# Optimization experiments

Measured on AMD Instinct MI355X. Metric: run time of the kernel, lower is better.

Reference implementation:

```python
import jax, jax.numpy as jnp
import numpy as np

HEADS = 12

def setup_inputs() -> dict:
    key = jax.random.key(0)
    ks = jax.random.split(key, 6)
    dim = 768
    x  = jax.random.normal(ks[0], (2, 4096, dim), dtype=jnp.float32)
    s = dim ** -0.5
    wq = jax.random.normal(ks[1], (dim, dim), dtype=jnp.float32) * s
    wk = jax.random.normal(ks[2], (dim, dim), dtype=jnp.float32) * s
    wv = jax.random.normal(ks[3], (dim, dim), dtype=jnp.float32) * s
    wo = jax.random.normal(ks[4], (dim, dim), dtype=jnp.float32) * s
    bo = jnp.zeros((dim,), dtype=jnp.float32)
    return {"x": x, "wq": wq, "wk": wk, "wv": wv, "wo": wo, "bo": bo}

def reference(x, wq, wk, wv, wo, bo):
    b, n, dim = x.shape
    h = HEADS
    d = dim // h
    scale = d ** -0.5
    # nn.Linear(dim, dim, bias=False): y = x @ W.T ; weights stored [out, in]
    def proj(w):
        return (x @ w.T).reshape(b, n, h, d).transpose(0, 2, 1, 3)  # b h n d
    q, k, v = proj(wq), proj(wk), proj(wv)
    dots = jnp.einsum('bhqd,bhkd->bhqk', q, k) * scale  # full N x N scores
    attn = jax.nn.softmax(dots, axis=-1)
    out = jnp.einsum('bhqk,bhkd->bhqd', attn, v)
    out = out.transpose(0, 2, 1, 3).reshape(b, n, dim)
    # to_out: Linear(dim, dim) + Dropout (identity at inference)
    return out @ wo.T + bo
```

## Files before the change

### kernel.cpp

```cpp
#include <hip/hip_runtime.h>
#include <hip/hip_bf16.h>


#define HEADS 12
#define NSEQ  4096
#define DIM   768
#define DH    64
#define BATCH 2
#define QSCALE 0.18033688f

typedef __attribute__((ext_vector_type(8))) short bf16x8;
typedef __attribute__((ext_vector_type(4))) float f32x4;
typedef __attribute__((ext_vector_type(4))) short bf16x4;

static __device__ __forceinline__ short f2bf(float f) {
    __hip_bfloat16 h = __float2bfloat16(f);
    return *reinterpret_cast<short*>(&h);
}

static __device__ __forceinline__ unsigned pkbf(float a, float b) {
    unsigned ua = __float_as_uint(a), ub = __float_as_uint(b);
    ua += 0x7FFFu + ((ua >> 16) & 1u);
    ub += 0x7FFFu + ((ub >> 16) & 1u);
    return __builtin_amdgcn_perm(ub, ua, 0x07060302);
}

#define GLL(g, l) __builtin_amdgcn_global_load_lds( \
    (const __attribute__((address_space(1))) void*)(g), \
    (__attribute__((address_space(3))) void*)(l), 16, 0, 0)

#define NX (BATCH*NSEQ*DIM)
#define NW (DIM*DIM)

__global__ __launch_bounds__(256) void convert_kernel(
    const float* __restrict__ x,  const float* __restrict__ wq,
    const float* __restrict__ wk, const float* __restrict__ wv,
    const float* __restrict__ wo,
    short* __restrict__ xb, short* __restrict__ wqb, short* __restrict__ wkb,
    short* __restrict__ wvb, short* __restrict__ wob)
{
    int i = (blockIdx.x * 256 + threadIdx.x) * 4;
    const float* src; short* dst; int off;
    if      (i < NX)          { src = x;  dst = xb;  off = i; }
    else if (i < NX + NW)     { src = wq; dst = wqb; off = i - NX; }
    else if (i < NX + 2*NW)   { src = wk; dst = wkb; off = i - NX - NW; }
    else if (i < NX + 3*NW)   { src = wv; dst = wvb; off = i - NX - 2*NW; }
    else                      { src = wo; dst = wob; off = i - NX - 3*NW; }
    float4 f = *(const float4*)(src + off);
    bf16x4 o; o[0] = f2bf(f.x); o[1] = f2bf(f.y); o[2] = f2bf(f.z); o[3] = f2bf(f.w);
    *(bf16x4*)(dst + off) = o;
}

__global__ __launch_bounds__(256, 4) void qkv_proj_kernel(
    const short* __restrict__ xb, const short* __restrict__ wqb,
    const short* __restrict__ wkb, const short* __restrict__ wvb,
    short* __restrict__ qb, short* __restrict__ kb, short* __restrict__ vtb)
{
    __shared__ __align__(16) short As[2][128*32];
    __shared__ __align__(16) short Bs[2][128*32];

    const int wave = threadIdx.x >> 6, lane = threadIdx.x & 63;
    const int lr = lane & 15, lq = lane >> 4;
    const int which = blockIdx.y / 6;
    const short* __restrict__ W = (which == 0) ? wqb : ((which == 1) ? wkb : wvb);
    const int m0  = blockIdx.x * 128;
    const int o0l = (blockIdx.y % 6) * 128;

    const short* __restrict__ gA = xb + (size_t)(m0  + wave*32 + (lane>>2)) * DIM + (lane&3)*8;
    const short* __restrict__ gB = W  + (size_t)(o0l + wave*32 + (lane>>2)) * DIM + (lane&3)*8;

    const int wm = (wave & 1) * 64, wn = (wave >> 1) * 64;

    f32x4 acc[4][4];
    #pragma unroll
    for (int i = 0; i < 4; i++)
        #pragma unroll
        for (int j = 0; j < 4; j++) acc[i][j] = (f32x4){0.f, 0.f, 0.f, 0.f};

    GLL(gA,            &As[0][(wave*32     )*32]);
    GLL(gA + 16*DIM,   &As[0][(wave*32 + 16)*32]);
    GLL(gB,            &Bs[0][(wave*32     )*32]);
    GLL(gB + 16*DIM,   &Bs[0][(wave*32 + 16)*32]);
    __syncthreads();

    for (int kt = 0; kt < 24; kt++) {
        const int p = kt & 1;
        if (kt < 23) {
            const int k1 = (kt + 1) * 32;
            GLL(gA + k1,          &As[1-p][(wave*32     )*32]);
            GLL(gA + k1 + 16*DIM, &As[1-p][(wave*32 + 16)*32]);
            GLL(gB + k1,          &Bs[1-p][(wave*32     )*32]);
            GLL(gB + k1 + 16*DIM, &Bs[1-p][(wave*32 + 16)*32]);
        }
        bf16x8 a[4], b[4];
        #pragma unroll
        for (int i = 0; i < 4; i++)
            a[i] = *(const bf16x8*)&As[p][(wm + i*16 + lr)*32 + lq*8];
        #pragma unroll
        for (int j = 0; j < 4; j++)
            b[j] = *(const bf16x8*)&Bs[p][(wn + j*16 + lr)*32 + lq*8];
        #pragma unroll
        for (int i = 0; i < 4; i++)
            #pragma unroll
            for (int j = 0; j < 4; j++)
                acc[i][j] = __builtin_amdgcn_mfma_f32_16x16x32_bf16(a[i], b[j], acc[i][j], 0, 0, 0);
        __syncthreads();
    }

    if (which == 2) {
        #pragma unroll
        for (int i = 0; i < 4; i++)
            #pragma unroll
            for (int j = 0; j < 4; j++) {
                const int mb = m0 + wm + i*16 + lq*4;
                const int o  = o0l + wn + j*16 + lr;
                const int bb = mb >> 12, n0 = mb & (NSEQ - 1);
                const int h  = o >> 6,   dd = o & 63;
                bf16x4 v;
                #pragma unroll
                for (int r = 0; r < 4; r++) v[r] = f2bf(acc[i][j][r]);
                *(bf16x4*)(vtb + ((size_t)(bb*HEADS + h) * DH + dd) * NSEQ + n0) = v;
            }
    } else {
        short* __restrict__ dst = (which == 0) ? qb : kb;
        const float scale = (which == 0) ? QSCALE : 1.0f;
        #pragma unroll
        for (int i = 0; i < 4; i++)
            #pragma unroll
            for (int j = 0; j < 4; j++)
                #pragma unroll
                for (int r = 0; r < 4; r++) {
                    const int m  = m0 + wm + i*16 + lq*4 + r;
                    const int o  = o0l + wn + j*16 + lr;
                    const int bb = m >> 12, n = m & (NSEQ - 1);
                    const int h  = o >> 6,  dd = o & 63;
                    dst[(((size_t)(bb*HEADS + h) * NSEQ) + n) * DH + dd] = f2bf(acc[i][j][r] * scale);
                }
    }
}

__global__ __launch_bounds__(256, 3) void attn_kernel(
    const short* __restrict__ qb, const short* __restrict__ kb,
    const short* __restrict__ vtb, short* __restrict__ ob)
{
    __shared__ __align__(16) short Ks[2][64*64];
    __shared__ __align__(16) short Vs[2][64*64];
    __shared__ __align__(16) short Vones[16*64];
    __shared__ __align__(16) short Ps[4][2][16*64];

    const int wave = threadIdx.x >> 6, lane = threadIdx.x & 63;
    const int lrow = lane & 15, lquad = lane >> 4;

    const int flat = blockIdx.x;
    const int xcd  = flat & 7;
    const int idx  = flat >> 3;
    const int bh   = xcd * 3 + (idx % 3);
    const int qblk = idx / 3;
    const int b = bh / HEADS, h = bh % HEADS;
    const int q0 = qblk * 128 + wave * 32;

    const short* __restrict__ Q  = qb  + (size_t)bh * NSEQ * DH;
    const short* __restrict__ K  = kb  + (size_t)bh * NSEQ * DH;
    const short* __restrict__ Vt = vtb + (size_t)bh * DH * NSEQ;

    for (int i = threadIdx.x; i < 16*64; i += 256) Vones[i] = 0x3F80;

    const int t  = threadIdx.x;
    const int r2 = t >> 3, cc = t & 7;
    const int ccs = (cc ^ (r2 & 7)) * 8;

    bf16x8 aq[2][2];
    #pragma unroll
    for (int rb = 0; rb < 2; rb++)
        #pragma unroll
        for (int kk = 0; kk < 2; kk++)
            aq[rb][kk] = *(const bf16x8*)(Q + (size_t)(q0 + rb*16 + lrow) * DH + kk*32 + lquad*8);

    f32x4 oacc[2][5];
    #pragma unroll
    for (int rb = 0; rb < 2; rb++)
        #pragma unroll
        for (int ct = 0; ct < 5; ct++) oacc[rb][ct] = (f32x4){0.f, 0.f, 0.f, 0.f};

    {
        bf16x8 k0a = *(const bf16x8*)(K  + (size_t)(r2     ) * DH   + cc*8);
        bf16x8 k0b = *(const bf16x8*)(K  + (size_t)(r2 + 32) * DH   + cc*8);
        bf16x8 v0a = *(const bf16x8*)(Vt + (size_t)(r2     ) * NSEQ + cc*8);
        bf16x8 v0b = *(const bf16x8*)(Vt + (size_t)(r2 + 32) * NSEQ + cc*8);
        *(bf16x8*)&Ks[0][ r2     *64 + ccs] = k0a;
        *(bf16x8*)&Ks[0][(r2+32) *64 + ccs] = k0b;
        *(bf16x8*)&Vs[0][ r2     *64 + ccs] = v0a;
        *(bf16x8*)&Vs[0][(r2+32) *64 + ccs] = v0b;
    }
    __syncthreads();

    bf16x8 bv4[2];
    #pragma unroll
    for (int kk = 0; kk < 2; kk++)
        bv4[kk] = *(const bf16x8*)&Vones[lrow*64 + (((kk*4 + lquad) ^ (lrow & 7)) * 8)];

    for (int kt = 0; kt < NSEQ / 64; kt++) {
        const int p = kt & 1;
        bf16x8 kr0, kr1, vr0, vr1;
        if (kt + 1 < NSEQ / 64) {
            const int key1 = (kt + 1) * 64;
            kr0 = *(const bf16x8*)(K  + (size_t)(key1 + r2     ) * DH   + cc*8);
            kr1 = *(const bf16x8*)(K  + (size_t)(key1 + r2 + 32) * DH   + cc*8);
            vr0 = *(const bf16x8*)(Vt + (size_t)(r2     ) * NSEQ + key1 + cc*8);
            vr1 = *(const bf16x8*)(Vt + (size_t)(r2 + 32) * NSEQ + key1 + cc*8);
        }

        bf16x8 ak[4][2];
        #pragma unroll
        for (int ct = 0; ct < 4; ct++)
            #pragma unroll
            for (int kk = 0; kk < 2; kk++)
                ak[ct][kk] = *(const bf16x8*)&Ks[p][(ct*16 + lrow)*64 + (((kk*4 + lquad) ^ (lrow & 7)) * 8)];

        #pragma unroll
        for (int rb = 0; rb < 2; rb++) {
            f32x4 s[4];
            #pragma unroll
            for (int ct = 0; ct < 4; ct++) s[ct] = (f32x4){0.f, 0.f, 0.f, 0.f};
            #pragma unroll
            for (int kk = 0; kk < 2; kk++)
                #pragma unroll
                for (int ct = 0; ct < 4; ct++)
                    s[ct] = __builtin_amdgcn_mfma_f32_16x16x32_bf16(ak[ct][kk], aq[rb][kk], s[ct], 0, 0, 0);
            #pragma unroll
            for (int ct = 0; ct < 4; ct++) {
                const float e0 = __builtin_amdgcn_exp2f(s[ct][0]);
                const float e1 = __builtin_amdgcn_exp2f(s[ct][1]);
                const float e2 = __builtin_amdgcn_exp2f(s[ct][2]);
                const float e3 = __builtin_amdgcn_exp2f(s[ct][3]);
                const unsigned lo = pkbf(e0, e1), hi = pkbf(e2, e3);
                const int cps = (((ct*2 + (lquad >> 1)) ^ (lrow & 7)) * 8) + (lquad & 1) * 4;
                *(uint2*)&Ps[wave][rb][lrow*64 + cps] = (uint2){lo, hi};
            }
        }

        bf16x8 bv[4][2];
        #pragma unroll
        for (int ct = 0; ct < 4; ct++)
            #pragma unroll
            for (int kk = 0; kk < 2; kk++)
                bv[ct][kk] = *(const bf16x8*)&Vs[p][(ct*16 + lrow)*64 + (((kk*4 + lquad) ^ (lrow & 7)) * 8)];

        #pragma unroll
        for (int rb = 0; rb < 2; rb++) {
            bf16x8 ap[2];
            #pragma unroll
            for (int kk = 0; kk < 2; kk++)
                ap[kk] = *(const bf16x8*)&Ps[wave][rb][lrow*64 + (((kk*4 + lquad) ^ (lrow & 7)) * 8)];
            #pragma unroll
            for (int kk = 0; kk < 2; kk++) {
                #pragma unroll
                for (int ct = 0; ct < 4; ct++)
                    oacc[rb][ct] = __builtin_amdgcn_mfma_f32_16x16x32_bf16(ap[kk], bv[ct][kk], oacc[rb][ct], 0, 0, 0);
                oacc[rb][4] = __builtin_amdgcn_mfma_f32_16x16x32_bf16(ap[kk], bv4[kk], oacc[rb][4], 0, 0, 0);
            }
        }

        if (kt + 1 < NSEQ / 64) {
            *(bf16x8*)&Ks[1-p][ r2     *64 + ccs] = kr0;
            *(bf16x8*)&Ks[1-p][(r2+32) *64 + ccs] = kr1;
            *(bf16x8*)&Vs[1-p][ r2     *64 + ccs] = vr0;
            *(bf16x8*)&Vs[1-p][(r2+32) *64 + ccs] = vr1;
        }
        __syncthreads();
    }

    #pragma unroll
    for (int rb = 0; rb < 2; rb++)
        #pragma unroll
        for (int r = 0; r < 4; r++) {
            const float inv = __builtin_amdgcn_rcpf(oacc[rb][4][r]);
            const int n = q0 + rb*16 + lquad*4 + r;
            #pragma unroll
            for (int ct = 0; ct < 4; ct++) {
                const int col = h*DH + ct*16 + lrow;
                ob[((size_t)b * NSEQ + n) * DIM + col] = f2bf(oacc[rb][ct][r] * inv);
            }
        }
}

__global__ __launch_bounds__(256, 4) void out_proj_kernel(
    const short* __restrict__ xo, const short* __restrict__ W,
    const float* __restrict__ bias, float* __restrict__ y)
{
    __shared__ __align__(16) short As[2][128*32];
    __shared__ __align__(16) short Bs[2][128*32];

    const int wave = threadIdx.x >> 6, lane = threadIdx.x & 63;
    const int lr = lane & 15, lq = lane >> 4;
    const int m0 = blockIdx.x * 128;
    const int o0 = blockIdx.y * 128;

    const short* __restrict__ gA = xo + (size_t)(m0 + wave*32 + (lane>>2)) * DIM + (lane&3)*8;
    const short* __restrict__ gB = W  + (size_t)(o0 + wave*32 + (lane>>2)) * DIM + (lane&3)*8;

    const int wm = (wave & 1) * 64, wn = (wave >> 1) * 64;

    f32x4 acc[4][4];
    #pragma unroll
    for (int i = 0; i < 4; i++)
        #pragma unroll
        for (int j = 0; j < 4; j++) acc[i][j] = (f32x4){0.f, 0.f, 0.f, 0.f};

    GLL(gA,            &As[0][(wave*32     )*32]);
    GLL(gA + 16*DIM,   &As[0][(wave*32 + 16)*32]);
    GLL(gB,            &Bs[0][(wave*32     )*32]);
    GLL(gB + 16*DIM,   &Bs[0][(wave*32 + 16)*32]);
    __syncthreads();

    for (int kt = 0; kt < 24; kt++) {
        const int p = kt & 1;
        if (kt < 23) {
            const int k1 = (kt + 1) * 32;
            GLL(gA + k1,          &As[1-p][(wave*32     )*32]);
            GLL(gA + k1 + 16*DIM, &As[1-p][(wave*32 + 16)*32]);
            GLL(gB + k1,          &Bs[1-p][(wave*32     )*32]);
            GLL(gB + k1 + 16*DIM, &Bs[1-p][(wave*32 + 16)*32]);
        }
        bf16x8 a[4], b[4];
        #pragma unroll
        for (int i = 0; i < 4; i++)
            a[i] = *(const bf16x8*)&As[p][(wm + i*16 + lr)*32 + lq*8];
        #pragma unroll
        for (int j = 0; j < 4; j++)
            b[j] = *(const bf16x8*)&Bs[p][(wn + j*16 + lr)*32 + lq*8];
        #pragma unroll
        for (int i = 0; i < 4; i++)
            #pragma unroll
            for (int j = 0; j < 4; j++)
                acc[i][j] = __builtin_amdgcn_mfma_f32_16x16x32_bf16(a[i], b[j], acc[i][j], 0, 0, 0);
        __syncthreads();
    }

    #pragma unroll
    for (int i = 0; i < 4; i++)
        #pragma unroll
        for (int j = 0; j < 4; j++)
            #pragma unroll
            for (int r = 0; r < 4; r++) {
                const int m = m0 + wm + i*16 + lq*4 + r;
                const int o = o0 + wn + j*16 + lr;
                y[(size_t)m * DIM + o] = acc[i][j][r] + bias[o];
            }
}

extern "C" void kernel_launch(void* const* d_in, const int* in_sizes, int n_in,
                              void* d_out, int out_size, void* d_ws, size_t ws_size,
                              hipStream_t stream) {
    const float* x  = (const float*)d_in[0];
    const float* wq = (const float*)d_in[1];
    const float* wk = (const float*)d_in[2];
    const float* wv = (const float*)d_in[3];
    const float* wo = (const float*)d_in[4];
    const float* bo = (const float*)d_in[5];
    float* out = (float*)d_out;

    const size_t qkv_elems = (size_t)BATCH * HEADS * NSEQ * DH;
    short* xb  = (short*)d_ws;
    short* wqb = xb  + NX;
    short* wkb = wqb + NW;
    short* wvb = wkb + NW;
    short* wob = wvb + NW;
    short* qb  = wob + NW;
    short* kb  = qb  + qkv_elems;
    short* vtb = kb  + qkv_elems;
    short* ob  = xb;

    dim3 blk(256);
    convert_kernel <<<dim3((NX + 4*NW) / 1024), blk, 0, stream>>>(x, wq, wk, wv, wo,
                                                                  xb, wqb, wkb, wvb, wob);
    qkv_proj_kernel<<<dim3(64, 18), blk, 0, stream>>>(xb, wqb, wkb, wvb, qb, kb, vtb);
    attn_kernel    <<<dim3(768), blk, 0, stream>>>(qb, kb, vtb, ob);
    out_proj_kernel<<<dim3(64, 6), blk, 0, stream>>>(ob, wob, bo, out);
}
```

Baseline: 280.9 us.

## Shrink attention tile to 16 query rows per wave and use hardware bf16 pack

Each wave in the attention kernel now handles 16 query rows instead of 32, so blocks cover 64 queries and the grid doubles to 1536 with a launch bound of 4 blocks per SM. The LDS ones-matrix is replaced by a register constant, and the software round-to-nearest bf16 packing is replaced by the v_cvt_pk_bf16_f32 instruction. The aim is more resident waves and less register and LDS pressure. The cost is that each K/V tile loaded into LDS is reused by half as many query rows, which doubles K/V global traffic and LDS reads per unit of work.

```diff
diff --git a/kernel.cpp b/kernel.cpp
--- a/kernel.cpp
+++ b/kernel.cpp
@@ -18,11 +18,10 @@
     return *reinterpret_cast<short*>(&h);
 }
 
-static __device__ __forceinline__ unsigned pkbf(float a, float b) {
-    unsigned ua = __float_as_uint(a), ub = __float_as_uint(b);
-    ua += 0x7FFFu + ((ua >> 16) & 1u);
-    ub += 0x7FFFu + ((ub >> 16) & 1u);
-    return __builtin_amdgcn_perm(ub, ua, 0x07060302);
+static __device__ __forceinline__ unsigned cvtpk(float a, float b) {
+    unsigned r;
+    asm("v_cvt_pk_bf16_f32 %0, %1, %2" : "=v"(r) : "v"(a), "v"(b));
+    return r;
 }
 
 #define GLL(g, l) __builtin_amdgcn_global_load_lds( \
@@ -139,14 +138,13 @@
     }
 }
 
-__global__ __launch_bounds__(256, 3) void attn_kernel(
+__global__ __launch_bounds__(256, 4) void attn_kernel(
     const short* __restrict__ qb, const short* __restrict__ kb,
     const short* __restrict__ vtb, short* __restrict__ ob)
 {
     __shared__ __align__(16) short Ks[2][64*64];
     __shared__ __align__(16) short Vs[2][64*64];
-    __shared__ __align__(16) short Vones[16*64];
-    __shared__ __align__(16) short Ps[4][2][16*64];
+    __shared__ __align__(16) short Ps[4][16*64];
 
     const int wave = threadIdx.x >> 6, lane = threadIdx.x & 63;
     const int lrow = lane & 15, lquad = lane >> 4;
@@ -157,30 +155,28 @@
     const int bh   = xcd * 3 + (idx % 3);
     const int qblk = idx / 3;
     const int b = bh / HEADS, h = bh % HEADS;
-    const int q0 = qblk * 128 + wave * 32;
+    const int q0 = qblk * 64 + wave * 16;
 
     const short* __restrict__ Q  = qb  + (size_t)bh * NSEQ * DH;
     const short* __restrict__ K  = kb  + (size_t)bh * NSEQ * DH;
     const short* __restrict__ Vt = vtb + (size_t)bh * DH * NSEQ;
 
-    for (int i = threadIdx.x; i < 16*64; i += 256) Vones[i] = 0x3F80;
-
     const int t  = threadIdx.x;
     const int r2 = t >> 3, cc = t & 7;
     const int ccs = (cc ^ (r2 & 7)) * 8;
 
-    bf16x8 aq[2][2];
-    #pragma unroll
-    for (int rb = 0; rb < 2; rb++)
-        #pragma unroll
-        for (int kk = 0; kk < 2; kk++)
-            aq[rb][kk] = *(const bf16x8*)(Q + (size_t)(q0 + rb*16 + lrow) * DH + kk*32 + lquad*8);
-
-    f32x4 oacc[2][5];
-    #pragma unroll
-    for (int rb = 0; rb < 2; rb++)
-        #pragma unroll
-        for (int ct = 0; ct < 5; ct++) oacc[rb][ct] = (f32x4){0.f, 0.f, 0.f, 0.f};
+    bf16x8 aq[2];
+    #pragma unroll
+    for (int kk = 0; kk < 2; kk++)
+        aq[kk] = *(const bf16x8*)(Q + (size_t)(q0 + lrow) * DH + kk*32 + lquad*8);
+
+    bf16x8 ones;
+    #pragma unroll
+    for (int i = 0; i < 8; i++) ones[i] = (short)0x3F80;
+
+    f32x4 oacc[5];
+    #pragma unroll
+    for (int ct = 0; ct < 5; ct++) oacc[ct] = (f32x4){0.f, 0.f, 0.f, 0.f};
 
     {
         bf16x8 k0a = *(const bf16x8*)(K  + (size_t)(r2     ) * DH   + cc*8);
@@ -194,11 +190,6 @@
     }
     __syncthreads();
 
-    bf16x8 bv4[2];
-    #pragma unroll
-    for (int kk = 0; kk < 2; kk++)
-        bv4[kk] = *(const bf16x8*)&Vones[lrow*64 + (((kk*4 + lquad) ^ (lrow & 7)) * 8)];
-
     for (int kt = 0; kt < NSEQ / 64; kt++) {
         const int p = kt & 1;
         bf16x8 kr0, kr1, vr0, vr1;
@@ -217,26 +208,24 @@
             for (int kk = 0; kk < 2; kk++)
                 ak[ct][kk] = *(const bf16x8*)&Ks[p][(ct*16 + lrow)*64 + (((kk*4 + lquad) ^ (lrow & 7)) * 8)];
 
-        #pragma unroll
-        for (int rb = 0; rb < 2; rb++) {
-            f32x4 s[4];
-            #pragma unroll
-            for (int ct = 0; ct < 4; ct++) s[ct] = (f32x4){0.f, 0.f, 0.f, 0.f};
-            #pragma unroll
-            for (int kk = 0; kk < 2; kk++)
-                #pragma unroll
-                for (int ct = 0; ct < 4; ct++)
-                    s[ct] = __builtin_amdgcn_mfma_f32_16x16x32_bf16(ak[ct][kk], aq[rb][kk], s[ct], 0, 0, 0);
-            #pragma unroll
-            for (int ct = 0; ct < 4; ct++) {
-                const float e0 = __builtin_amdgcn_exp2f(s[ct][0]);
-                const float e1 = __builtin_amdgcn_exp2f(s[ct][1]);
-                const float e2 = __builtin_amdgcn_exp2f(s[ct][2]);
-                const float e3 = __builtin_amdgcn_exp2f(s[ct][3]);
-                const unsigned lo = pkbf(e0, e1), hi = pkbf(e2, e3);
-                const int cps = (((ct*2 + (lquad >> 1)) ^ (lrow & 7)) * 8) + (lquad & 1) * 4;
-                *(uint2*)&Ps[wave][rb][lrow*64 + cps] = (uint2){lo, hi};
-            }
+        f32x4 s[4];
+        #pragma unroll
+        for (int ct = 0; ct < 4; ct++) s[ct] = (f32x4){0.f, 0.f, 0.f, 0.f};
+        #pragma unroll
+        for (int kk = 0; kk < 2; kk++)
+            #pragma unroll
+            for (int ct = 0; ct < 4; ct++)
+                s[ct] = __builtin_amdgcn_mfma_f32_16x16x32_bf16(ak[ct][kk], aq[kk], s[ct], 0, 0, 0);
+
+        #pragma unroll
+        for (int ct = 0; ct < 4; ct++) {
+            const float e0 = __builtin_amdgcn_exp2f(s[ct][0]);
+            const float e1 = __builtin_amdgcn_exp2f(s[ct][1]);
+            const float e2 = __builtin_amdgcn_exp2f(s[ct][2]);
+            const float e3 = __builtin_amdgcn_exp2f(s[ct][3]);
+            const unsigned lo = cvtpk(e0, e1), hi = cvtpk(e2, e3);
+            const int cps = (((ct*2 + (lquad >> 1)) ^ (lrow & 7)) * 8) + (lquad & 1) * 4;
+            *(uint2*)&Ps[wave][lrow*64 + cps] = (uint2){lo, hi};
         }
 
         bf16x8 bv[4][2];
@@ -246,19 +235,17 @@
             for (int kk = 0; kk < 2; kk++)
                 bv[ct][kk] = *(const bf16x8*)&Vs[p][(ct*16 + lrow)*64 + (((kk*4 + lquad) ^ (lrow & 7)) * 8)];
 
-        #pragma unroll
-        for (int rb = 0; rb < 2; rb++) {
-            bf16x8 ap[2];
-            #pragma unroll
-            for (int kk = 0; kk < 2; kk++)
-                ap[kk] = *(const bf16x8*)&Ps[wave][rb][lrow*64 + (((kk*4 + lquad) ^ (lrow & 7)) * 8)];
-            #pragma unroll
-            for (int kk = 0; kk < 2; kk++) {
-                #pragma unroll
-                for (int ct = 0; ct < 4; ct++)
-                    oacc[rb][ct] = __builtin_amdgcn_mfma_f32_16x16x32_bf16(ap[kk], bv[ct][kk], oacc[rb][ct], 0, 0, 0);
-                oacc[rb][4] = __builtin_amdgcn_mfma_f32_16x16x32_bf16(ap[kk], bv4[kk], oacc[rb][4], 0, 0, 0);
-            }
+        bf16x8 ap[2];
+        #pragma unroll
+        for (int kk = 0; kk < 2; kk++)
+            ap[kk] = *(const bf16x8*)&Ps[wave][lrow*64 + (((kk*4 + lquad) ^ (lrow & 7)) * 8)];
+
+        #pragma unroll
+        for (int kk = 0; kk < 2; kk++) {
+            #pragma unroll
+            for (int ct = 0; ct < 4; ct++)
+                oacc[ct] = __builtin_amdgcn_mfma_f32_16x16x32_bf16(ap[kk], bv[ct][kk], oacc[ct], 0, 0, 0);
+            oacc[4] = __builtin_amdgcn_mfma_f32_16x16x32_bf16(ap[kk], ones, oacc[4], 0, 0, 0);
         }
 
         if (kt + 1 < NSEQ / 64) {
@@ -271,17 +258,15 @@
     }
 
     #pragma unroll
-    for (int rb = 0; rb < 2; rb++)
-        #pragma unroll
-        for (int r = 0; r < 4; r++) {
-            const float inv = __builtin_amdgcn_rcpf(oacc[rb][4][r]);
-            const int n = q0 + rb*16 + lquad*4 + r;
-            #pragma unroll
-            for (int ct = 0; ct < 4; ct++) {
-                const int col = h*DH + ct*16 + lrow;
-                ob[((size_t)b * NSEQ + n) * DIM + col] = f2bf(oacc[rb][ct][r] * inv);
-            }
-        }
+    for (int r = 0; r < 4; r++) {
+        const float inv = __builtin_amdgcn_rcpf(oacc[4][r]);
+        const int n = q0 + lquad*4 + r;
+        #pragma unroll
+        for (int ct = 0; ct < 4; ct++) {
+            const int col = h*DH + ct*16 + lrow;
+            ob[((size_t)b * NSEQ + n) * DIM + col] = f2bf(oacc[ct][r] * inv);
+        }
+    }
 }
 
 __global__ __launch_bounds__(256, 4) void out_proj_kernel(
@@ -375,6 +360,6 @@
     convert_kernel <<<dim3((NX + 4*NW) / 1024), blk, 0, stream>>>(x, wq, wk, wv, wo,
                                                                   xb, wqb, wkb, wvb, wob);
     qkv_proj_kernel<<<dim3(64, 18), blk, 0, stream>>>(xb, wqb, wkb, wvb, qb, kb, vtb);
-    attn_kernel    <<<dim3(768), blk, 0, stream>>>(qb, kb, vtb, ob);
+    attn_kernel    <<<dim3(1536), blk, 0, stream>>>(qb, kb, vtb, ob);
     out_proj_kernel<<<dim3(64, 6), blk, 0, stream>>>(ob, wob, bo, out);
 }
```

Measured after the change: 292.7 us. +4.2%, slower.
